# Kernel tuning notes

Measured on AMD Instinct MI355X. Metric: run time of the kernel, lower is better.

Reference implementation:

```python
import jax, jax.numpy as jnp
import numpy as np
from math import sqrt

B, LT, LM = 4, 512, 1024
HID, NH, HD = 512, 8, 64          # self-attn: hidden, n_head, head_size
NHP, KS = 16, 64                  # cross-attn: 2*max_charge*n_head_per_mass, key_size
FF = 4 * HID
ALPHA = 2.0
EPS = 1e-5


def apply_rope(x, dis):
    # dis: same trailing dim as x; chunk into (sin, cos) halves
    s, c = jnp.split(dis, 2, axis=-1)
    x0, x1 = x[..., 0::2], x[..., 1::2]
    return jnp.concatenate([x0 * c - x1 * s, x1 * c + x0 * s], axis=-1)


def layer_norm(x, g, b):
    mu = jnp.mean(x, axis=-1, keepdims=True)
    var = jnp.mean(jnp.square(x - mu), axis=-1, keepdims=True)
    return (x - mu) * jax.lax.rsqrt(var + EPS) * g + b


def deep_norm(x, postx, g, b):
    # dropout is identity in eval mode
    return layer_norm(x * ALPHA + postx, g, b)


def attn_block(x_q, x_kv, dis_q, dis_k, wq, bq, wk, bk, wv, bv, wo, bo, mask, n_head, head_size):
    bsz = x_q.shape[0]
    q = (x_q @ wq.T + bq).reshape(bsz, -1, n_head, head_size)
    k = (x_kv @ wk.T + bk).reshape(bsz, -1, n_head, head_size)
    v = (x_kv @ wv.T + bv).reshape(bsz, -1, n_head, head_size)
    q = apply_rope(q, dis_q)
    k = apply_rope(k, dis_k)
    attn = jnp.einsum('bnhd,bmhd->bhnm', q, k) / sqrt(head_size)  # [B,H,Lq,Lk]
    attn = jnp.where(mask, attn, -jnp.inf)
    attn = jax.nn.softmax(attn, axis=-1)
    out = jnp.einsum('bhnm,bmhd->bnhd', attn, v).reshape(bsz, -1, n_head * head_size)
    return out @ wo.T + bo


def setup_inputs() -> dict:
    key = jax.random.key(0)
    ks = jax.random.split(key, 32)
    rn = lambda i, shape, s=1.0: jax.random.normal(ks[i], shape, jnp.float32) * s
    inp = {}
    inp['tgt'] = rn(0, (B, LT, HID))
    inp['mem'] = rn(1, (B, LM, HID))
    inp['glycan_mass'] = rn(2, (B, LT, NH, HD))
    inp['glycan_query_mass'] = rn(3, (B, LT, NH, HD))
    inp['glycan_crossattn_mass'] = rn(4, (B, LT, NHP, KS))
    inp['node_mass_emb'] = rn(5, (B, LM, NHP, KS))
    inp['node_mass'] = rn(6, (B, LM))
    causal = jnp.tril(jnp.ones((LT, LT), bool))
    inp['tgt_mask'] = jnp.broadcast_to(causal[None, None], (B, 1, LT, LT))
    inp['rel_mask'] = jnp.ones((B, 1, LT, LM), bool)
    inp['layer'] = 0
    inp['A'] = rn(7, (1,))
    w = 0.03  # param init scale
    # self-attn params
    inp['wq1'] = rn(8, (HID, HID), w);  inp['bq1'] = jnp.zeros((HID,))
    inp['wk1'] = rn(9, (HID, HID), w);  inp['bk1'] = jnp.zeros((HID,))
    inp['wv1'] = rn(10, (HID, HID), w); inp['bv1'] = jnp.zeros((HID,))
    inp['wo1'] = rn(11, (HID, HID), w); inp['bo1'] = jnp.zeros((HID,))
    inp['ln1_g'] = jnp.ones((HID,));    inp['ln1_b'] = jnp.zeros((HID,))
    # cross-attn params (projection dim NHP*KS = 1024)
    P = NHP * KS
    inp['wq2'] = rn(12, (P, HID), w);   inp['bq2'] = jnp.zeros((P,))
    inp['wk2'] = rn(13, (P, HID), w);   inp['bk2'] = jnp.zeros((P,))
    inp['wv2'] = rn(14, (P, HID), w);   inp['bv2'] = jnp.zeros((P,))
    inp['wo2'] = rn(15, (HID, P), w);   inp['bo2'] = jnp.zeros((HID,))
    inp['ln2_g'] = jnp.ones((HID,));    inp['ln2_b'] = jnp.zeros((HID,))
    # FFN params (no bias) + DeepNorm LN
    inp['w_ff1'] = rn(16, (FF, HID), w)
    inp['w_ff2'] = rn(17, (HID, FF), w)
    inp['ln3_g'] = jnp.ones((HID,));    inp['ln3_b'] = jnp.zeros((HID,))
    return inp


def reference(tgt, mem, glycan_mass, glycan_query_mass, glycan_crossattn_mass,
              node_mass_emb, node_mass, tgt_mask, rel_mask, layer, A,
              wq1, bq1, wk1, bk1, wv1, bv1, wo1, bo1, ln1_g, ln1_b,
              wq2, bq2, wk2, bk2, wv2, bv2, wo2, bo2, ln2_g, ln2_b,
              w_ff1, w_ff2, ln3_g, ln3_b):
    # masked self-attention with mass RoPE + DeepNorm
    postx = attn_block(tgt, tgt, glycan_query_mass, glycan_mass,
                       wq1, bq1, wk1, bk1, wv1, bv1, wo1, bo1,
                       tgt_mask, NH, HD)
    tgt = deep_norm(tgt, postx, ln1_g, ln1_b)
    # cross-attention with mass RoPE + DeepNorm (node_mass, layer, A unused in math)
    postx = attn_block(tgt, mem, glycan_crossattn_mass, node_mass_emb,
                       wq2, bq2, wk2, bk2, wv2, bv2, wo2, bo2,
                       rel_mask, NHP, KS)
    tgt = deep_norm(tgt, postx, ln2_g, ln2_b)
    # FFN + DeepNorm
    postx = jax.nn.relu(tgt @ w_ff1.T) @ w_ff2.T
    tgt = deep_norm(tgt, postx, ln3_g, ln3_b)
    return (tgt, A)
```

## Files before the change

kernel.cpp:

```cpp
#include <hip/hip_runtime.h>
#include <hip/hip_bf16.h>
#include <math.h>

#define EPS 1e-5f

typedef __attribute__((ext_vector_type(8))) __bf16 bf16x8;
typedef __attribute__((ext_vector_type(4))) float f32x4;

struct CvtJobs {
    const float* src[12];
    __bf16* dst[12];
    int off[13];
};

__global__ __launch_bounds__(256) void cvt_k(CvtJobs J, int total) {
    int g = blockIdx.x * 256 + threadIdx.x;
    if (g >= total) return;
    int j = 0;
    #pragma unroll
    for (int t = 0; t < 11; ++t) j += (g >= J.off[t + 1]) ? 1 : 0;
    int lg = g - J.off[j];
    const float* s = J.src[j] + (size_t)lg * 8;
    float4 a = *(const float4*)s;
    float4 b = *(const float4*)(s + 4);
    bf16x8 o;
    o[0] = (__bf16)a.x; o[1] = (__bf16)a.y; o[2] = (__bf16)a.z; o[3] = (__bf16)a.w;
    o[4] = (__bf16)b.x; o[5] = (__bf16)b.y; o[6] = (__bf16)b.z; o[7] = (__bf16)b.w;
    *(bf16x8*)(J.dst[j] + (size_t)lg * 8) = o;
}

template<int BT, int KS, typename OutT, bool RELU, bool HAS_BIAS>
__global__ __launch_bounds__(256) void gemm_bf16_k(const __bf16* __restrict__ A,
                                                   const __bf16* __restrict__ W,
                                                   const float* __restrict__ b0,
                                                   const float* __restrict__ b1,
                                                   const float* __restrict__ b2,
                                                   int bshift,
                                                   OutT* __restrict__ C,
                                                   int M, int N, int K) {
    constexpr int NI = BT / 32;
    __shared__ __bf16 As[BT * 64];
    __shared__ __bf16 Ws[BT * 64];

    const int tid  = threadIdx.x;
    const int wave = tid >> 6;
    const int lane = tid & 63;
    const int frow = lane & 15;
    const int fgrp = lane >> 4;

    const int nb  = gridDim.x * gridDim.y;
    const int bid = blockIdx.y * gridDim.x + blockIdx.x;
    const int v   = (bid & 7) * (nb >> 3) + (bid >> 3);
    const int bx  = (v % gridDim.x) * BT;
    const int by  = (v / gridDim.x) * BT;

    const int Kc = K / KS;
    const int kbeg = blockIdx.z * Kc;
    OutT* Cz = C + (size_t)blockIdx.z * M * N;

    const int wr = (wave >> 1) * (BT / 2);
    const int wc = (wave & 1) * (BT / 2);
    const int ldr = lane >> 3;
    const int ldc = (lane & 7) * 8;

    f32x4 acc[NI][NI] = {};

    for (int k0 = kbeg; k0 < kbeg + Kc; k0 += 64) {
        #pragma unroll
        for (int it = 0; it < NI; ++it) {
            int chunk = it * 4 + wave;
            int r = chunk * 8 + ldr;
            const __bf16* ga = A + (size_t)(by + r) * K + k0 + ldc;
            const __bf16* gw = W + (size_t)(bx + r) * K + k0 + ldc;
            __builtin_amdgcn_global_load_lds(
                (const __attribute__((address_space(1))) unsigned int*)ga,
                (__attribute__((address_space(3))) unsigned int*)(As + chunk * 512),
                16, 0, 0);
            __builtin_amdgcn_global_load_lds(
                (const __attribute__((address_space(1))) unsigned int*)gw,
                (__attribute__((address_space(3))) unsigned int*)(Ws + chunk * 512),
                16, 0, 0);
        }
        __syncthreads();

        #pragma unroll
        for (int kk = 0; kk < 2; ++kk) {
            bf16x8 af[NI], wf[NI];
            #pragma unroll
            for (int i = 0; i < NI; ++i)
                af[i] = *(const bf16x8*)&As[(wr + i * 16 + frow) * 64 + kk * 32 + fgrp * 8];
            #pragma unroll
            for (int j = 0; j < NI; ++j)
                wf[j] = *(const bf16x8*)&Ws[(wc + j * 16 + frow) * 64 + kk * 32 + fgrp * 8];
            #pragma unroll
            for (int i = 0; i < NI; ++i)
                #pragma unroll
                for (int j = 0; j < NI; ++j)
                    acc[i][j] = __builtin_amdgcn_mfma_f32_16x16x32_bf16(af[i], wf[j], acc[i][j], 0, 0, 0);
        }
        __syncthreads();
    }

    #pragma unroll
    for (int i = 0; i < NI; ++i) {
        #pragma unroll
        for (int jj = 0; jj < 4; ++jj) {
            int row = by + wr + i * 16 + fgrp * 4 + jj;
            #pragma unroll
            for (int j = 0; j < NI; ++j) {
                int col = bx + wc + j * 16 + frow;
                float val = acc[i][j][jj];
                if (HAS_BIAS) {
                    int sel = col >> bshift;
                    const float* bp = sel == 0 ? b0 : (sel == 1 ? b1 : b2);
                    val += bp[col & (int)((1u << bshift) - 1)];
                }
                if (RELU) val = fmaxf(val, 0.0f);
                Cz[(size_t)row * N + col] = (OutT)val;
            }
        }
    }
}

__global__ __launch_bounds__(256) void rope_bf16_k(__bf16* __restrict__ x,
                                                   const float* __restrict__ dis,
                                                   int rows, int hshift, int rowstride) {
    int r = blockIdx.x * 256 + threadIdx.x;
    if (r >= rows) return;
    int h = r & ((1 << hshift) - 1);
    int rt = r >> hshift;
    __bf16* xr = x + (size_t)rt * rowstride + h * 64;
    const float* d = dis + (size_t)r * 64;
    float xv[64];
    #pragma unroll
    for (int j = 0; j < 8; ++j) {
        bf16x8 vv = *(const bf16x8*)(xr + j * 8);
        #pragma unroll
        for (int t = 0; t < 8; ++t) xv[j * 8 + t] = (float)vv[t];
    }
    float ov[64];
    #pragma unroll
    for (int j = 0; j < 32; ++j) {
        float s = d[j], c = d[32 + j];
        float x0 = xv[2 * j], x1 = xv[2 * j + 1];
        ov[j]      = x0 * c - x1 * s;
        ov[32 + j] = x1 * c + x0 * s;
    }
    #pragma unroll
    for (int j = 0; j < 8; ++j) {
        bf16x8 vv;
        #pragma unroll
        for (int t = 0; t < 8; ++t) vv[t] = (__bf16)ov[j * 8 + t];
        *(bf16x8*)(xr + j * 8) = vv;
    }
}

template<bool CAUSAL, int NSPLIT>
__global__ __launch_bounds__(256) void attn_bf16_k(const __bf16* __restrict__ Q,
                                                   const __bf16* __restrict__ K,
                                                   const __bf16* __restrict__ V,
                                                   const float* __restrict__ disQ,
                                                   __bf16* __restrict__ Opart,
                                                   float* __restrict__ lsums,
                                                   int H, int LQ, int LM,
                                                   int qstride, int kvstride,
                                                   int prows) {
    __shared__ __bf16 Ks[64 * 72];
    __shared__ __bf16 Vt[64 * 72];
    __shared__ __bf16 Ps[4 * 16 * 72];

    const int nqt = LQ >> 6;
    const int nb  = gridDim.x;
    const int bid = blockIdx.x;
    const int v   = (bid & 7) * (nb >> 3) + (bid >> 3);
    int t = v;
    const int qt = t % nqt; t /= nqt;
    const int chunk = t % NSPLIT; t /= NSPLIT;
    const int h = t % H;
    const int b = t / H;
    const int q0 = qt * 64;

    const int tid  = threadIdx.x;
    const int wave = tid >> 6;
    const int lane = tid & 63;
    const int frow = lane & 15;
    const int fgrp = lane >> 4;

    const int qrow = q0 + wave * 16 + frow;
    bf16x8 qf0, qf1;
    {
        const __bf16* qp = Q + ((size_t)b * LQ + qrow) * qstride + h * 64 + fgrp * 16;
        bf16x8 xa = *(const bf16x8*)qp;
        bf16x8 xb = *(const bf16x8*)(qp + 8);
        float xs[16];
        #pragma unroll
        for (int u = 0; u < 8; ++u) { xs[u] = (float)xa[u]; xs[8 + u] = (float)xb[u]; }
        const float* dq = disQ + (((size_t)b * LQ + qrow) * H + h) * 64 + fgrp * 8;
        #pragma unroll
        for (int u = 0; u < 8; ++u) {
            float sv = dq[u], cv = dq[32 + u];
            float x0 = xs[2 * u], x1 = xs[2 * u + 1];
            qf0[u] = (__bf16)(x0 * cv - x1 * sv);
            qf1[u] = (__bf16)(x1 * cv + x0 * sv);
        }
    }

    f32x4 oacc[4] = {};
    float lsum[4] = {};

    const int kbAll = CAUSAL ? (qt + 1) : (LM >> 6);
    const int kcnt  = (LM >> 6) / NSPLIT;
    const int kb0   = chunk * kcnt;
    const int kb1   = min(kbAll, kb0 + kcnt);

    const int r   = tid >> 2;
    const int c0q = tid & 3;
    const int kphys = (r & 7) + 8 * ((r >> 3) ^ (2 * c0q));

    for (int kb = kb0; kb < kb1; ++kb) {
        const int m0 = kb * 64;
        {
            const __bf16* kp = K + ((size_t)b * LM + m0 + r) * kvstride + h * 64 + c0q * 16;
            *(bf16x8*)&Ks[r * 72 + c0q * 16]     = *(const bf16x8*)kp;
            *(bf16x8*)&Ks[r * 72 + c0q * 16 + 8] = *(const bf16x8*)(kp + 8);
        }
        {
            const __bf16* vp = V + ((size_t)b * LM + m0 + r) * kvstride + h * 64 + c0q * 16;
            bf16x8 va = *(const bf16x8*)vp;
            bf16x8 vb = *(const bf16x8*)(vp + 8);
            #pragma unroll
            for (int j = 0; j < 8; ++j) {
                Vt[(c0q * 16 + j) * 72 + kphys]     = va[j];
                Vt[(c0q * 16 + 8 + j) * 72 + kphys] = vb[j];
            }
        }
        __syncthreads();

        f32x4 s[4];
        #pragma unroll
        for (int n = 0; n < 4; ++n) {
            bf16x8 kf0 = *(const bf16x8*)&Ks[(n * 16 + frow) * 72 + fgrp * 8];
            bf16x8 kf1 = *(const bf16x8*)&Ks[(n * 16 + frow) * 72 + 32 + fgrp * 8];
            f32x4 tt = {0.f, 0.f, 0.f, 0.f};
            tt = __builtin_amdgcn_mfma_f32_16x16x32_bf16(qf0, kf0, tt, 0, 0, 0);
            tt = __builtin_amdgcn_mfma_f32_16x16x32_bf16(qf1, kf1, tt, 0, 0, 0);
            s[n] = tt;
        }

        #pragma unroll
        for (int n = 0; n < 4; ++n)
            #pragma unroll
            for (int jj = 0; jj < 4; ++jj) {
                bool valid = (!CAUSAL) ||
                    ((m0 + n * 16 + frow) <= (q0 + wave * 16 + fgrp * 4 + jj));
                s[n][jj] = valid ? __expf(s[n][jj] * 0.125f - 8.0f) : 0.0f;
            }

        #pragma unroll
        for (int jj = 0; jj < 4; ++jj) {
            float rs = (s[0][jj] + s[1][jj]) + (s[2][jj] + s[3][jj]);
            #pragma unroll
            for (int msk = 8; msk >= 1; msk >>= 1) rs += __shfl_xor(rs, msk);
            lsum[jj] += rs;
        }

        #pragma unroll
        for (int n = 0; n < 4; ++n)
            #pragma unroll
            for (int jj = 0; jj < 4; ++jj) {
                int q = fgrp * 4 + jj;
                int kidx = (frow & 7) + 8 * (((2 * n) + (frow >> 3)) ^ (2 * ((q >> 3) & 1)));
                Ps[wave * 1152 + q * 72 + kidx] = (__bf16)s[n][jj];
            }

        #pragma unroll
        for (int c = 0; c < 2; ++c) {
            int pblk = (c * 4 + fgrp) ^ (2 * ((frow >> 3) & 1));
            bf16x8 pf = *(const bf16x8*)&Ps[wave * 1152 + frow * 72 + 8 * pblk];
            #pragma unroll
            for (int n = 0; n < 4; ++n) {
                int vblk = (c * 4 + fgrp) ^ (2 * n);
                bf16x8 vf = *(const bf16x8*)&Vt[(n * 16 + frow) * 72 + 8 * vblk];
                oacc[n] = __builtin_amdgcn_mfma_f32_16x16x32_bf16(pf, vf, oacc[n], 0, 0, 0);
            }
        }
        __syncthreads();
    }

    #pragma unroll
    for (int jj = 0; jj < 4; ++jj) {
        int q = q0 + wave * 16 + fgrp * 4 + jj;
        size_t ridx = (size_t)chunk * prows + ((size_t)b * LQ + q) * H + h;
        if (frow == 0) lsums[ridx] = lsum[jj];
        #pragma unroll
        for (int n = 0; n < 4; ++n)
            Opart[ridx * 64 + n * 16 + frow] = (__bf16)oacc[n][jj];
    }
}

template<int NS>
__global__ __launch_bounds__(256) void attn_merge_k(const __bf16* __restrict__ Opart,
                                                    const float* __restrict__ lsums,
                                                    __bf16* __restrict__ O,
                                                    int rows, int H, int ostride) {
    int rid = blockIdx.x * 4 + (threadIdx.x >> 6);
    int lane = threadIdx.x & 63;
    float den = 0.f, acc = 0.f;
    #pragma unroll
    for (int i = 0; i < NS; ++i) {
        den += lsums[(size_t)i * rows + rid];
        acc += (float)Opart[((size_t)i * rows + rid) * 64 + lane];
    }
    int h = rid % H, bq = rid / H;
    O[(size_t)bq * ostride + h * 64 + lane] = (__bf16)(acc / den);
}

template<int NP, bool HASB, bool WRITE_BF>
__global__ __launch_bounds__(256) void deepnorm_k(const float* __restrict__ x,
                                                  const float* __restrict__ p0,
                                                  const float* __restrict__ p1,
                                                  const float* __restrict__ p2,
                                                  const float* __restrict__ p3,
                                                  const float* __restrict__ bias,
                                                  const float* __restrict__ g,
                                                  const float* __restrict__ b,
                                                  float* __restrict__ out,
                                                  __bf16* __restrict__ out_bf) {
    int row = blockIdx.x;
    int tid = threadIdx.x;
    size_t i0 = (size_t)row * 512 + tid, i1 = i0 + 256;
    float a0 = p0[i0], a1 = p0[i1];
    if (NP > 1) { a0 += p1[i0]; a1 += p1[i1]; }
    if (NP > 2) { a0 += p2[i0]; a1 += p2[i1]; }
    if (NP > 3) { a0 += p3[i0]; a1 += p3[i1]; }
    if (HASB)   { a0 += bias[tid]; a1 += bias[tid + 256]; }
    float v0 = x[i0] * 2.0f + a0;
    float v1 = x[i1] * 2.0f + a1;

    __shared__ float red[4];
    int wave = tid >> 6, lane = tid & 63;

    float s = v0 + v1;
    #pragma unroll
    for (int o = 32; o >= 1; o >>= 1) s += __shfl_xor(s, o);
    if (lane == 0) red[wave] = s;
    __syncthreads();
    float mean = (red[0] + red[1] + red[2] + red[3]) * (1.0f / 512.0f);

    float d0 = v0 - mean, d1 = v1 - mean;
    float vs = d0 * d0 + d1 * d1;
    #pragma unroll
    for (int o = 32; o >= 1; o >>= 1) vs += __shfl_xor(vs, o);
    __syncthreads();
    if (lane == 0) red[wave] = vs;
    __syncthreads();
    float var = (red[0] + red[1] + red[2] + red[3]) * (1.0f / 512.0f);
    float inv = rsqrtf(var + EPS);

    float o0 = d0 * inv * g[tid] + b[tid];
    float o1 = d1 * inv * g[tid + 256] + b[tid + 256];
    out[i0] = o0;
    out[i1] = o1;
    if (WRITE_BF) {
        out_bf[i0] = (__bf16)o0;
        out_bf[i1] = (__bf16)o1;
    }
}

__global__ void copy_a_k(const float* __restrict__ A, float* __restrict__ out) {
    out[0] = A[0];
}

extern "C" void kernel_launch(void* const* d_in, const int* in_sizes, int n_in,
                              void* d_out, int out_size, void* d_ws, size_t ws_size,
                              hipStream_t stream) {
    const float* tgt  = (const float*)d_in[0];
    const float* mem  = (const float*)d_in[1];
    const float* dis_k1 = (const float*)d_in[2];
    const float* dis_q1 = (const float*)d_in[3];
    const float* dis_q2 = (const float*)d_in[4];
    const float* dis_k2 = (const float*)d_in[5];
    const float* A_in   = (const float*)d_in[10];
    const float* wq1 = (const float*)d_in[11]; const float* bq1 = (const float*)d_in[12];
    const float* wk1 = (const float*)d_in[13]; const float* bk1 = (const float*)d_in[14];
    const float* wv1 = (const float*)d_in[15]; const float* bv1 = (const float*)d_in[16];
    const float* wo1 = (const float*)d_in[17]; const float* bo1 = (const float*)d_in[18];
    const float* ln1g = (const float*)d_in[19]; const float* ln1b = (const float*)d_in[20];
    const float* wq2 = (const float*)d_in[21]; const float* bq2 = (const float*)d_in[22];
    const float* wk2 = (const float*)d_in[23]; const float* bk2 = (const float*)d_in[24];
    const float* wv2 = (const float*)d_in[25]; const float* bv2 = (const float*)d_in[26];
    const float* wo2 = (const float*)d_in[27]; const float* bo2 = (const float*)d_in[28];
    const float* ln2g = (const float*)d_in[29]; const float* ln2b = (const float*)d_in[30];
    const float* wff1 = (const float*)d_in[31]; const float* wff2 = (const float*)d_in[32];
    const float* ln3g = (const float*)d_in[33]; const float* ln3b = (const float*)d_in[34];

    char* ws = (char*)d_ws;
    auto MB = [&](size_t mb) { return ws + mb * 1024 * 1024; };

    __bf16* wqkv1_bf = (__bf16*)MB(0);
    __bf16* wo1_bf   = (__bf16*)MB(2);
    __bf16* wq2_bf   = (__bf16*)MB(3);
    __bf16* wkv2_bf  = (__bf16*)MB(4);
    __bf16* wo2_bf   = (__bf16*)MB(6);
    __bf16* wff1_bf  = (__bf16*)MB(7);
    __bf16* wff2_bf  = (__bf16*)MB(9);
    __bf16* tgt_bf   = (__bf16*)MB(11);
    __bf16* mem_bf   = (__bf16*)MB(13);
    __bf16* qkv1_bf  = (__bf16*)MB(17);
    __bf16* att1_bf  = (__bf16*)MB(23);
    float*  post0    = (float*)MB(25);
    float*  post1    = (float*)MB(29);
    float*  post2    = (float*)MB(33);
    float*  post3    = (float*)MB(37);
    float*  x1       = (float*)MB(41);
    __bf16* kv2_bf   = (__bf16*)MB(45);
    __bf16* att2_bf  = (__bf16*)MB(61);
    float*  x2       = (float*)MB(65);
    __bf16* x2_bf    = (__bf16*)MB(69);
    float*  lsums    = (float*)MB(71);
    __bf16* Opart    = (__bf16*)MB(25);
    __bf16* x1_bf    = tgt_bf;
    __bf16* q2_bf    = qkv1_bf;
    __bf16* ffh_bf   = kv2_bf;

    float* out = (float*)d_out;

    CvtJobs J;
    const float* srcs[12] = {tgt, mem, wq1, wk1, wv1, wo1, wq2, wk2, wv2, wo2, wff1, wff2};
    __bf16* dsts[12] = {tgt_bf, mem_bf, wqkv1_bf, wqkv1_bf + 262144, wqkv1_bf + 524288,
                        wo1_bf, wq2_bf, wkv2_bf, wkv2_bf + 524288, wo2_bf, wff1_bf, wff2_bf};
    int sizes[12] = {2048 * 512, 4096 * 512, 512 * 512, 512 * 512, 512 * 512, 512 * 512,
                     1024 * 512, 1024 * 512, 1024 * 512, 1024 * 512, 2048 * 512, 512 * 2048};
    int acc = 0;
    for (int i = 0; i < 12; ++i) { J.src[i] = srcs[i]; J.dst[i] = dsts[i]; J.off[i] = acc; acc += sizes[i] / 8; }
    J.off[12] = acc;
    cvt_k<<<(acc + 255) / 256, 256, 0, stream>>>(J, acc);

    gemm_bf16_k<64, 1, __bf16, false, true><<<dim3(24, 32), 256, 0, stream>>>(
        tgt_bf, wqkv1_bf, bq1, bk1, bv1, 9, qkv1_bf, 2048, 1536, 512);
    rope_bf16_k<<<64, 256, 0, stream>>>(qkv1_bf + 512, dis_k1, 16384, 3, 1536);
    attn_bf16_k<true, 2><<<512, 256, 0, stream>>>(qkv1_bf, qkv1_bf + 512, qkv1_bf + 1024,
                                                  dis_q1, Opart, lsums,
                                                  8, 512, 512, 1536, 1536, 16384);
    attn_merge_k<2><<<4096, 256, 0, stream>>>(Opart, lsums, att1_bf, 16384, 8, 512);
    gemm_bf16_k<64, 2, float, false, false><<<dim3(8, 32, 2), 256, 0, stream>>>(
        att1_bf, wo1_bf, nullptr, nullptr, nullptr, 31, post0, 2048, 512, 512);
    deepnorm_k<2, true, true><<<2048, 256, 0, stream>>>(tgt, post0, post1, nullptr, nullptr,
                                                        bo1, ln1g, ln1b, x1, x1_bf);

    gemm_bf16_k<64, 1, __bf16, false, true><<<dim3(16, 32), 256, 0, stream>>>(
        x1_bf, wq2_bf, bq2, bq2, bq2, 31, q2_bf, 2048, 1024, 512);
    gemm_bf16_k<128, 1, __bf16, false, true><<<dim3(16, 32), 256, 0, stream>>>(
        mem_bf, wkv2_bf, bk2, bv2, bv2, 10, kv2_bf, 4096, 2048, 512);
    rope_bf16_k<<<256, 256, 0, stream>>>(kv2_bf, dis_k2, 65536, 4, 2048);
    attn_bf16_k<false, 2><<<1024, 256, 0, stream>>>(q2_bf, kv2_bf, kv2_bf + 1024,
                                                    dis_q2, Opart, lsums,
                                                    16, 512, 1024, 1024, 2048, 32768);
    attn_merge_k<2><<<8192, 256, 0, stream>>>(Opart, lsums, att2_bf, 32768, 16, 1024);
    gemm_bf16_k<64, 2, float, false, false><<<dim3(8, 32, 2), 256, 0, stream>>>(
        att2_bf, wo2_bf, nullptr, nullptr, nullptr, 31, post0, 2048, 512, 1024);
    deepnorm_k<2, true, true><<<2048, 256, 0, stream>>>(x1, post0, post1, nullptr, nullptr,
                                                        bo2, ln2g, ln2b, x2, x2_bf);

    gemm_bf16_k<64, 1, __bf16, true, false><<<dim3(32, 32), 256, 0, stream>>>(
        x2_bf, wff1_bf, nullptr, nullptr, nullptr, 31, ffh_bf, 2048, 2048, 512);
    gemm_bf16_k<64, 4, float, false, false><<<dim3(8, 32, 4), 256, 0, stream>>>(
        ffh_bf, wff2_bf, nullptr, nullptr, nullptr, 31, post0, 2048, 512, 2048);
    deepnorm_k<4, false, false><<<2048, 256, 0, stream>>>(x2, post0, post1, post2, post3,
                                                          nullptr, ln3g, ln3b, out, nullptr);

    copy_a_k<<<1, 1, 0, stream>>>(A_in, out + 2048 * 512);
}
```

Measured before the change: 186.8 us.

## Fuse RoPE into QKV GEMM epilogue and attention merge into Wo GEMM

After: 187.2 us. About the same (+0.2%).

```diff
diff --git a/kernel.cpp b/kernel.cpp
--- a/kernel.cpp
+++ b/kernel.cpp
@@ -29,13 +29,15 @@
     *(bf16x8*)(J.dst[j] + (size_t)lg * 8) = o;
 }
 
-template<int BT, int KS, typename OutT, bool RELU, bool HAS_BIAS>
+template<int BT, int KS, typename OutT, bool RELU, bool HAS_BIAS, bool ROPE>
 __global__ __launch_bounds__(256) void gemm_bf16_k(const __bf16* __restrict__ A,
                                                    const __bf16* __restrict__ W,
                                                    const float* __restrict__ b0,
                                                    const float* __restrict__ b1,
                                                    const float* __restrict__ b2,
                                                    int bshift,
+                                                   const float* __restrict__ disK,
+                                                   int ropeLo, int ropeHi, int dstride,
                                                    OutT* __restrict__ C,
                                                    int M, int N, int K) {
     constexpr int NI = BT / 32;
@@ -116,43 +118,108 @@
                     val += bp[col & (int)((1u << bshift) - 1)];
                 }
                 if (RELU) val = fmaxf(val, 0.0f);
-                Cz[(size_t)row * N + col] = (OutT)val;
+                int colw = col;
+                if (ROPE && col >= ropeLo && col < ropeHi) {
+                    int hcol = col & 63;
+                    int jr = hcol >> 1;
+                    int hbase = col - hcol;
+                    const float* dr = disK + (size_t)row * dstride + (hbase - ropeLo);
+                    float sv = dr[jr], cv = dr[32 + jr];
+                    float pv = __shfl_xor(val, 1);
+                    if ((col & 1) == 0) { val = val * cv - pv * sv; colw = hbase + jr; }
+                    else                { val = val * cv + pv * sv; colw = hbase + 32 + jr; }
+                }
+                Cz[(size_t)row * N + colw] = (OutT)val;
             }
         }
     }
 }
 
-__global__ __launch_bounds__(256) void rope_bf16_k(__bf16* __restrict__ x,
-                                                   const float* __restrict__ dis,
-                                                   int rows, int hshift, int rowstride) {
-    int r = blockIdx.x * 256 + threadIdx.x;
-    if (r >= rows) return;
-    int h = r & ((1 << hshift) - 1);
-    int rt = r >> hshift;
-    __bf16* xr = x + (size_t)rt * rowstride + h * 64;
-    const float* d = dis + (size_t)r * 64;
-    float xv[64];
+template<int KS>
+__global__ __launch_bounds__(256) void gemm_wo_k(const __bf16* __restrict__ Opart,
+                                                 const float* __restrict__ lsums,
+                                                 int prows, int H,
+                                                 const __bf16* __restrict__ W,
+                                                 float* __restrict__ C,
+                                                 int M, int N, int K) {
+    __shared__ __bf16 As[64 * 64];
+    __shared__ __bf16 Ws[64 * 64];
+
+    const int tid  = threadIdx.x;
+    const int wave = tid >> 6;
+    const int lane = tid & 63;
+    const int frow = lane & 15;
+    const int fgrp = lane >> 4;
+
+    const int nb  = gridDim.x * gridDim.y;
+    const int bid = blockIdx.y * gridDim.x + blockIdx.x;
+    const int v   = (bid & 7) * (nb >> 3) + (bid >> 3);
+    const int bx  = (v % gridDim.x) * 64;
+    const int by  = (v / gridDim.x) * 64;
+
+    const int Kc = K / KS;
+    const int kbeg = blockIdx.z * Kc;
+    float* Cz = C + (size_t)blockIdx.z * M * N;
+
+    const int wr = (wave >> 1) * 32;
+    const int wc = (wave & 1) * 32;
+    const int ldr = lane >> 3;
+    const int ldc = (lane & 7) * 8;
+
+    f32x4 acc[2][2] = {};
+
+    for (int k0 = kbeg; k0 < kbeg + Kc; k0 += 64) {
+        const int h = k0 >> 6;
+        #pragma unroll
+        for (int it = 0; it < 2; ++it) {
+            int chunk = it * 4 + wave;
+            int r = chunk * 8 + ldr;
+            size_t rid = (size_t)(by + r) * H + h;
+            bf16x8 o0 = *(const bf16x8*)&Opart[rid * 64 + ldc];
+            bf16x8 o1 = *(const bf16x8*)&Opart[((size_t)prows + rid) * 64 + ldc];
+            float li = 1.0f / (lsums[rid] + lsums[prows + rid]);
+            bf16x8 m;
+            #pragma unroll
+            for (int u = 0; u < 8; ++u)
+                m[u] = (__bf16)(((float)o0[u] + (float)o1[u]) * li);
+            *(bf16x8*)&As[chunk * 512 + lane * 8] = m;
+            const __bf16* gw = W + (size_t)(bx + r) * K + k0 + ldc;
+            __builtin_amdgcn_global_load_lds(
+                (const __attribute__((address_space(1))) unsigned int*)gw,
+                (__attribute__((address_space(3))) unsigned int*)(Ws + chunk * 512),
+                16, 0, 0);
+        }
+        __syncthreads();
+
+        #pragma unroll
+        for (int kk = 0; kk < 2; ++kk) {
+            bf16x8 af[2], wf[2];
+            #pragma unroll
+            for (int i = 0; i < 2; ++i)
+                af[i] = *(const bf16x8*)&As[(wr + i * 16 + frow) * 64 + kk * 32 + fgrp * 8];
+            #pragma unroll
+            for (int j = 0; j < 2; ++j)
+                wf[j] = *(const bf16x8*)&Ws[(wc + j * 16 + frow) * 64 + kk * 32 + fgrp * 8];
+            #pragma unroll
+            for (int i = 0; i < 2; ++i)
+                #pragma unroll
+                for (int j = 0; j < 2; ++j)
+                    acc[i][j] = __builtin_amdgcn_mfma_f32_16x16x32_bf16(af[i], wf[j], acc[i][j], 0, 0, 0);
+        }
+        __syncthreads();
+    }
+
     #pragma unroll
-    for (int j = 0; j < 8; ++j) {
-        bf16x8 vv = *(const bf16x8*)(xr + j * 8);
-        #pragma unroll
-        for (int t = 0; t < 8; ++t) xv[j * 8 + t] = (float)vv[t];
-    }
-    float ov[64];
-    #pragma unroll
-    for (int j = 0; j < 32; ++j) {
-        float s = d[j], c = d[32 + j];
-        float x0 = xv[2 * j], x1 = xv[2 * j + 1];
-        ov[j]      = x0 * c - x1 * s;
-        ov[32 + j] = x1 * c + x0 * s;
-    }
-    #pragma unroll
-    for (int j = 0; j < 8; ++j) {
-        bf16x8 vv;
-        #pragma unroll
-        for (int t = 0; t < 8; ++t) vv[t] = (__bf16)ov[j * 8 + t];
-        *(bf16x8*)(xr + j * 8) = vv;
-    }
+    for (int i = 0; i < 2; ++i)
+        #pragma unroll
+        for (int jj = 0; jj < 4; ++jj) {
+            int row = by + wr + i * 16 + fgrp * 4 + jj;
+            #pragma unroll
+            for (int j = 0; j < 2; ++j) {
+                int col = bx + wc + j * 16 + frow;
+                Cz[(size_t)row * N + col] = acc[i][j][jj];
+            }
+        }
 }
 
 template<bool CAUSAL, int NSPLIT>
@@ -298,23 +365,6 @@
     }
 }
 
-template<int NS>
-__global__ __launch_bounds__(256) void attn_merge_k(const __bf16* __restrict__ Opart,
-                                                    const float* __restrict__ lsums,
-                                                    __bf16* __restrict__ O,
-                                                    int rows, int H, int ostride) {
-    int rid = blockIdx.x * 4 + (threadIdx.x >> 6);
-    int lane = threadIdx.x & 63;
-    float den = 0.f, acc = 0.f;
-    #pragma unroll
-    for (int i = 0; i < NS; ++i) {
-        den += lsums[(size_t)i * rows + rid];
-        acc += (float)Opart[((size_t)i * rows + rid) * 64 + lane];
-    }
-    int h = rid % H, bq = rid / H;
-    O[(size_t)bq * ostride + h * 64 + lane] = (__bf16)(acc / den);
-}
-
 template<int NP, bool HASB, bool WRITE_BF>
 __global__ __launch_bounds__(256) void deepnorm_k(const float* __restrict__ x,
                                                   const float* __restrict__ p0,
@@ -325,9 +375,12 @@
                                                   const float* __restrict__ g,
                                                   const float* __restrict__ b,
                                                   float* __restrict__ out,
-                                                  __bf16* __restrict__ out_bf) {
+                                                  __bf16* __restrict__ out_bf,
+                                                  const float* __restrict__ Ain,
+                                                  float* __restrict__ Aout) {
     int row = blockIdx.x;
     int tid = threadIdx.x;
+    if (Aout && row == 0 && tid == 0) Aout[0] = Ain[0];
     size_t i0 = (size_t)row * 512 + tid, i1 = i0 + 256;
     float a0 = p0[i0], a1 = p0[i1];
     if (NP > 1) { a0 += p1[i0]; a1 += p1[i1]; }
@@ -365,10 +418,6 @@
         out_bf[i0] = (__bf16)o0;
         out_bf[i1] = (__bf16)o1;
     }
-}
-
-__global__ void copy_a_k(const float* __restrict__ A, float* __restrict__ out) {
-    out[0] = A[0];
 }
 
 extern "C" void kernel_launch(void* const* d_in, const int* in_sizes, int n_in,
@@ -407,21 +456,19 @@
     __bf16* tgt_bf   = (__bf16*)MB(11);
     __bf16* mem_bf   = (__bf16*)MB(13);
     __bf16* qkv1_bf  = (__bf16*)MB(17);
-    __bf16* att1_bf  = (__bf16*)MB(23);
-    float*  post0    = (float*)MB(25);
-    float*  post1    = (float*)MB(29);
-    float*  post2    = (float*)MB(33);
-    float*  post3    = (float*)MB(37);
+    __bf16* Opart    = (__bf16*)MB(25);
     float*  x1       = (float*)MB(41);
+    float*  post0    = (float*)MB(45);
+    float*  post1    = (float*)MB(49);
+    float*  post2    = (float*)MB(53);
+    float*  post3    = (float*)MB(57);
     __bf16* kv2_bf   = (__bf16*)MB(45);
-    __bf16* att2_bf  = (__bf16*)MB(61);
     float*  x2       = (float*)MB(65);
     __bf16* x2_bf    = (__bf16*)MB(69);
     float*  lsums    = (float*)MB(71);
-    __bf16* Opart    = (__bf16*)MB(25);
     __bf16* x1_bf    = tgt_bf;
     __bf16* q2_bf    = qkv1_bf;
-    __bf16* ffh_bf   = kv2_bf;
+    __bf16* ffh_bf   = Opart;
 
     float* out = (float*)d_out;
 
@@ -436,38 +483,41 @@
     J.off[12] = acc;
     cvt_k<<<(acc + 255) / 256, 256, 0, stream>>>(J, acc);
 
-    gemm_bf16_k<64, 1, __bf16, false, true><<<dim3(24, 32), 256, 0, stream>>>(
-        tgt_bf, wqkv1_bf, bq1, bk1, bv1, 9, qkv1_bf, 2048, 1536, 512);
-    rope_bf16_k<<<64, 256, 0, stream>>>(qkv1_bf + 512, dis_k1, 16384, 3, 1536);
+
+    gemm_bf16_k<64, 1, __bf16, false, true, true><<<dim3(24, 32), 256, 0, stream>>>(
+        tgt_bf, wqkv1_bf, bq1, bk1, bv1, 9, dis_k1, 512, 1024, 512,
+        qkv1_bf, 2048, 1536, 512);
     attn_bf16_k<true, 2><<<512, 256, 0, stream>>>(qkv1_bf, qkv1_bf + 512, qkv1_bf + 1024,
                                                   dis_q1, Opart, lsums,
                                                   8, 512, 512, 1536, 1536, 16384);
-    attn_merge_k<2><<<4096, 256, 0, stream>>>(Opart, lsums, att1_bf, 16384, 8, 512);
-    gemm_bf16_k<64, 2, float, false, false><<<dim3(8, 32, 2), 256, 0, stream>>>(
-        att1_bf, wo1_bf, nullptr, nullptr, nullptr, 31, post0, 2048, 512, 512);
+    gemm_wo_k<2><<<dim3(8, 32, 2), 256, 0, stream>>>(Opart, lsums, 16384, 8,
+                                                     wo1_bf, post0, 2048, 512, 512);
     deepnorm_k<2, true, true><<<2048, 256, 0, stream>>>(tgt, post0, post1, nullptr, nullptr,
-                                                        bo1, ln1g, ln1b, x1, x1_bf);
-
-    gemm_bf16_k<64, 1, __bf16, false, true><<<dim3(16, 32), 256, 0, stream>>>(
-        x1_bf, wq2_bf, bq2, bq2, bq2, 31, q2_bf, 2048, 1024, 512);
-    gemm_bf16_k<128, 1, __bf16, false, true><<<dim3(16, 32), 256, 0, stream>>>(
-        mem_bf, wkv2_bf, bk2, bv2, bv2, 10, kv2_bf, 4096, 2048, 512);
-    rope_bf16_k<<<256, 256, 0, stream>>>(kv2_bf, dis_k2, 65536, 4, 2048);
+                                                        bo1, ln1g, ln1b, x1, x1_bf,
+                                                        nullptr, nullptr);
+
+    gemm_bf16_k<64, 1, __bf16, false, true, false><<<dim3(16, 32), 256, 0, stream>>>(
+        x1_bf, wq2_bf, bq2, bq2, bq2, 31, nullptr, 0, 0, 0,
+        q2_bf, 2048, 1024, 512);
+    gemm_bf16_k<128, 1, __bf16, false, true, true><<<dim3(16, 32), 256, 0, stream>>>(
+        mem_bf, wkv2_bf, bk2, bv2, bv2, 10, dis_k2, 0, 1024, 1024,
+        kv2_bf, 4096, 2048, 512);
     attn_bf16_k<false, 2><<<1024, 256, 0, stream>>>(q2_bf, kv2_bf, kv2_bf + 1024,
                                                     dis_q2, Opart, lsums,
                                                     16, 512, 1024, 1024, 2048, 32768);
-    attn_merge_k<2><<<8192, 256, 0, stream>>>(Opart, lsums, att2_bf, 32768, 16, 1024);
-    gemm_bf16_k<64, 2, float, false, false><<<dim3(8, 32, 2), 256, 0, stream>>>(
-        att2_bf, wo2_bf, nullptr, nullptr, nullptr, 31, post0, 2048, 512, 1024);
+    gemm_wo_k<2><<<dim3(8, 32, 2), 256, 0, stream>>>(Opart, lsums, 32768, 16,
+                                                     wo2_bf, post0, 2048, 512, 1024);
     deepnorm_k<2, true, true><<<2048, 256, 0, stream>>>(x1, post0, post1, nullptr, nullptr,
-                                                        bo2, ln2g, ln2b, x2, x2_bf);
-
-    gemm_bf16_k<64, 1, __bf16, true, false><<<dim3(32, 32), 256, 0, stream>>>(
-        x2_bf, wff1_bf, nullptr, nullptr, nullptr, 31, ffh_bf, 2048, 2048, 512);
-    gemm_bf16_k<64, 4, float, false, false><<<dim3(8, 32, 4), 256, 0, stream>>>(
-        ffh_bf, wff2_bf, nullptr, nullptr, nullptr, 31, post0, 2048, 512, 2048);
+                                                        bo2, ln2g, ln2b, x2, x2_bf,
+                                                        nullptr, nullptr);
+
+    gemm_bf16_k<64, 1, __bf16, true, false, false><<<dim3(32, 32), 256, 0, stream>>>(
+        x2_bf, wff1_bf, nullptr, nullptr, nullptr, 31, nullptr, 0, 0, 0,
+        ffh_bf, 2048, 2048, 512);
+    gemm_bf16_k<64, 4, float, false, false, false><<<dim3(8, 32, 4), 256, 0, stream>>>(
+        ffh_bf, wff2_bf, nullptr, nullptr, nullptr, 31, nullptr, 0, 0, 0,
+        post0, 2048, 512, 2048);
     deepnorm_k<4, false, false><<<2048, 256, 0, stream>>>(x2, post0, post1, post2, post3,
-                                                          nullptr, ln3g, ln3b, out, nullptr);
-
-    copy_a_k<<<1, 1, 0, stream>>>(A_in, out + 2048 * 512);
+                                                          nullptr, ln3g, ln3b, out, nullptr,
+                                                          A_in, out + 2048 * 512);
 }
```
